# Performance work log

Hardware: AMD Instinct MI355X
Metric: run time of the kernel (lower is better)

Reference implementation:

```python
import jax, jax.numpy as jnp
import numpy as np

B, H, W, C = 8, 64, 64, 64


def setup_inputs() -> dict:
    key = jax.random.key(0)
    ks = jax.random.split(key, 9)
    s = 1.0 / np.sqrt(C)
    return {
        "x": jax.random.normal(ks[0], (B, H, W, C), dtype=jnp.float32),
        "wq": jax.random.uniform(ks[1], (C, C), jnp.float32, -s, s),
        "bq": jax.random.uniform(ks[2], (C,), jnp.float32, -s, s),
        "wk": jax.random.uniform(ks[3], (C, C), jnp.float32, -s, s),
        "bk": jax.random.uniform(ks[4], (C,), jnp.float32, -s, s),
        "wv": jax.random.uniform(ks[5], (C, C), jnp.float32, -s, s),
        "bv": jax.random.uniform(ks[6], (C,), jnp.float32, -s, s),
        "wp": jax.random.uniform(ks[7], (C, C), jnp.float32, -s, s),
        "bp": jax.random.uniform(ks[8], (C,), jnp.float32, -s, s),
    }


def reference(x, wq, bq, wk, bk, wv, bv, wp, bp):
    b, h, w, c = x.shape
    n = h * w
    xf = x.reshape(b, n, c)
    scale = c ** (-0.5)
    q = xf @ wq.T + bq  # [B,N,C]
    k = xf @ wk.T + bk
    v = xf @ wv.T + bv
    center_idx = (h // 2) * w + (w // 2)
    central = q[:, center_idx, :][:, None, :]           # [B,1,C]
    qb = jnp.broadcast_to(central, (b, n, c))           # rank-1 broadcast query
    pos = jnp.arange(n)
    dist = jnp.sqrt(((pos // w - h // 2) ** 2 + (pos % w - w // 2) ** 2).astype(jnp.float32))
    weights = jnp.exp(1.0 - dist)                       # [N]
    qw = qb * weights[None, :, None]
    attn = jnp.einsum('bnc,bmc->bnm', qw, k) * scale    # dense [B,N,N] (memory-bound)
    attn = jax.nn.softmax(attn, axis=-1)
    out = jnp.einsum('bnm,bmc->bnc', attn, v)
    out = out @ wp.T + bp
    return out.reshape(b, h, w, c)
```

## Files before the change

kernel.cpp:

```cpp
#include <hip/hip_runtime.h>

#define BB 8
#define NN 4096
#define CC 64
#define CENTER (32*64 + 32)
#define MS 64
#define RR (NN/MS)
#define GE 32
#define XPAD 68
#define CUT 64

struct Geom {
    short gid[2049];
    short g2d2[64];
    int ng;
};

constexpr Geom makeGeom() {
    Geom t{};
    bool occ[2049] = {};
    for (int y = 0; y < 64; ++y)
        for (int x = 0; x < 64; ++x) {
            int dy = y - 32, dx = x - 32;
            occ[dy*dy + dx*dx] = true;
        }
    int g = 0;
    for (int i = 0; i < CUT; ++i) {
        if (occ[i]) { t.gid[i] = (short)g; t.g2d2[g] = (short)i; ++g; }
        else t.gid[i] = (short)-1;
    }
    t.ng = g;
    for (int i = CUT; i <= 2048; ++i) t.gid[i] = occ[i] ? (short)g : (short)-1;
    return t;
}

constexpr int NGN = makeGeom().ng;
static_assert(NGN + 1 <= GE, "group padding");
static_assert(GE == 32, "decode assumes GE=32");
static_assert(MS * RR == NN, "geometry");
__constant__ Geom GEOM = makeGeom();

constexpr int OFF_PART = 0;
constexpr int OFF_ZP   = OFF_PART + BB*MS*GE*CC;
constexpr int OFF_OG   = OFF_ZP + BB*MS*GE;

#define FMA4(A, E, V) do { (A).x += (E)*(V).x; (A).y += (E)*(V).y; \
                           (A).z += (E)*(V).z; (A).w += (E)*(V).w; } while(0)

__global__ __launch_bounds__(256) void k_main(
    const float* __restrict__ x,
    const float* __restrict__ wq, const float* __restrict__ bq,
    const float* __restrict__ wk, const float* __restrict__ bk,
    float* __restrict__ part, float* __restrict__ zpart)
{
    __shared__ __align__(16) float xs[RR*XPAD];
    __shared__ float qs[CC];
    __shared__ float us[CC];
    __shared__ __align__(16) float ss[RR];
    __shared__ float ts_s;

    const int tid = threadIdx.x;
    const int b   = blockIdx.x & 7;
    const int ms  = blockIdx.x >> 3;
    const int m0  = ms * RR;

    float4 xr[4];
    const float4* x4 = (const float4*)x + ((size_t)b*NN + m0)*16;
    #pragma unroll
    for (int k = 0; k < 4; ++k) xr[k] = x4[tid + 256*k];

    if (tid < CC) {
        const float* xc = x + ((size_t)b*NN + CENTER)*CC;
        const float* wr = wq + tid*CC;
        float a0 = bq[tid], a1 = 0.f, a2 = 0.f, a3 = 0.f;
        #pragma unroll
        for (int i = 0; i < CC; i += 4) {
            a0 += xc[i+0]*wr[i+0]; a1 += xc[i+1]*wr[i+1];
            a2 += xc[i+2]*wr[i+2]; a3 += xc[i+3]*wr[i+3];
        }
        qs[tid] = a0+a1+a2+a3;
    }
    #pragma unroll
    for (int k = 0; k < 4; ++k) {
        const int idx = tid + 256*k;
        *(float4*)&xs[(idx >> 4)*XPAD + (idx & 15)*4] = xr[k];
    }
    __syncthreads();

    if (tid < CC) {
        float a0=0.f,a1=0.f,a2=0.f,a3=0.f;
        #pragma unroll
        for (int j = 0; j < CC; j += 4) {
            a0 += qs[j+0]*wk[(j+0)*CC + tid];
            a1 += qs[j+1]*wk[(j+1)*CC + tid];
            a2 += qs[j+2]*wk[(j+2)*CC + tid];
            a3 += qs[j+3]*wk[(j+3)*CC + tid];
        }
        us[tid] = a0+a1+a2+a3;
    } else if (tid == CC) {
        float a = 0.f;
        for (int j = 0; j < CC; ++j) a += qs[j]*bk[j];
        ts_s = a;
    }
    __syncthreads();

    if (tid < 2*RR) {
        const int r = tid >> 1, h = tid & 1;
        const float* xrow = &xs[r*XPAD + h*32];
        const float* uh = &us[h*32];
        float a0=0.f,a1=0.f,a2=0.f,a3=0.f;
        #pragma unroll
        for (int i = 0; i < 32; i += 4) {
            a0 += xrow[i+0]*uh[i+0]; a1 += xrow[i+1]*uh[i+1];
            a2 += xrow[i+2]*uh[i+2]; a3 += xrow[i+3]*uh[i+3];
        }
        float p = a0+a1+a2+a3;
        p += __shfl_xor(p, 1, 64);
        if (h == 0) ss[r] = (p + ts_s) * 0.125f;
    }
    __syncthreads();

    const int g  = tid >> 3;
    const int i0 = (tid & 7) * 8;
    const float wg = (g < NGN) ? __expf(1.f - sqrtf((float)GEOM.g2d2[g])) : 0.f;
    float4 y0 = make_float4(0.f,0.f,0.f,0.f), y1 = make_float4(0.f,0.f,0.f,0.f);
    float z = 0.f;
    #pragma unroll 4
    for (int r4 = 0; r4 < RR; r4 += 4) {
        const float4 s4 = *(const float4*)&ss[r4];
        float e;
        e = __expf(wg*s4.x); z += e;
        FMA4(y0, e, *(const float4*)&xs[(r4+0)*XPAD + i0]);
        FMA4(y1, e, *(const float4*)&xs[(r4+0)*XPAD + i0 + 4]);
        e = __expf(wg*s4.y); z += e;
        FMA4(y0, e, *(const float4*)&xs[(r4+1)*XPAD + i0]);
        FMA4(y1, e, *(const float4*)&xs[(r4+1)*XPAD + i0 + 4]);
        e = __expf(wg*s4.z); z += e;
        FMA4(y0, e, *(const float4*)&xs[(r4+2)*XPAD + i0]);
        FMA4(y1, e, *(const float4*)&xs[(r4+2)*XPAD + i0 + 4]);
        e = __expf(wg*s4.w); z += e;
        FMA4(y0, e, *(const float4*)&xs[(r4+3)*XPAD + i0]);
        FMA4(y1, e, *(const float4*)&xs[(r4+3)*XPAD + i0 + 4]);
    }
    float4* p4 = (float4*)part + ((size_t)((b*MS + ms)*GE + g)*CC + i0)/4;
    p4[0] = y0; p4[1] = y1;
    if ((tid & 7) == 0) zpart[(b*MS + ms)*GE + g] = z;
}

__global__ __launch_bounds__(256) void k_final(
    const float* __restrict__ part, const float* __restrict__ zpart,
    const float* __restrict__ wv, const float* __restrict__ bv,
    const float* __restrict__ wp, const float* __restrict__ bp,
    float* __restrict__ og)
{
    __shared__ float yred[4*CC];
    __shared__ float ysh[CC];
    __shared__ float hsh[CC];
    __shared__ float zsh;

    const int tid = threadIdx.x;
    const int b = blockIdx.x >> 5, g = blockIdx.x & 31;
    const int i = tid & 63, q = tid >> 6;

    float a = 0.f;
    #pragma unroll
    for (int j = 0; j < MS/4; ++j) {
        const int ms = q*(MS/4) + j;
        a += part[((size_t)(b*MS + ms)*GE + g)*CC + i];
    }
    yred[q*CC + i] = a;

    float zv = 0.f;
    if (tid < 64) {
        zv = zpart[(b*MS + tid)*GE + g];
        zv += __shfl_xor(zv, 1, 64);
        zv += __shfl_xor(zv, 2, 64);
        zv += __shfl_xor(zv, 4, 64);
        zv += __shfl_xor(zv, 8, 64);
        zv += __shfl_xor(zv, 16, 64);
        zv += __shfl_xor(zv, 32, 64);
        if (tid == 0) zsh = zv;
    }
    __syncthreads();
    if (tid < CC)
        ysh[tid] = yred[tid] + yred[CC+tid] + yred[2*CC+tid] + yred[3*CC+tid];
    __syncthreads();
    if (tid < CC) {
        const float* wr = wv + tid*CC;
        float a0=0.f,a1=0.f,a2=0.f,a3=0.f;
        #pragma unroll
        for (int j = 0; j < CC; j += 4) {
            a0 += wr[j+0]*ysh[j+0]; a1 += wr[j+1]*ysh[j+1];
            a2 += wr[j+2]*ysh[j+2]; a3 += wr[j+3]*ysh[j+3];
        }
        hsh[tid] = (a0+a1+a2+a3)/zsh + bv[tid];
    }
    __syncthreads();
    if (tid < CC) {
        const float* wr = wp + tid*CC;
        float a0=bp[tid],a1=0.f,a2=0.f,a3=0.f;
        #pragma unroll
        for (int j = 0; j < CC; j += 4) {
            a0 += wr[j+0]*hsh[j+0]; a1 += wr[j+1]*hsh[j+1];
            a2 += wr[j+2]*hsh[j+2]; a3 += wr[j+3]*hsh[j+3];
        }
        og[((size_t)b*GE + g)*CC + tid] = a0+a1+a2+a3;
    }
}

__global__ __launch_bounds__(256) void k_out(
    const float* __restrict__ og, float* __restrict__ out)
{
    const int i4 = blockIdx.x * 256 + threadIdx.x;
    const int c4 = i4 & 15;
    const int n  = (i4 >> 4) & (NN - 1);
    const int bb = i4 >> 16;
    const int dy = (n >> 6) - 32, dx = (n & 63) - 32;
    const int g  = GEOM.gid[dy*dy + dx*dx];
    ((float4*)out)[i4] = ((const float4*)og)[(size_t)(bb*GE + g)*16 + c4];
}

extern "C" void kernel_launch(void* const* d_in, const int* in_sizes, int n_in,
                              void* d_out, int out_size, void* d_ws, size_t ws_size,
                              hipStream_t stream) {
    const float* x  = (const float*)d_in[0];
    const float* wq = (const float*)d_in[1];
    const float* bq = (const float*)d_in[2];
    const float* wk = (const float*)d_in[3];
    const float* bk = (const float*)d_in[4];
    const float* wv = (const float*)d_in[5];
    const float* bv = (const float*)d_in[6];
    const float* wp = (const float*)d_in[7];
    const float* bp = (const float*)d_in[8];
    float* ws = (float*)d_ws;

    k_main<<<MS*8, 256, 0, stream>>>(x, wq, bq, wk, bk,
                                     ws + OFF_PART, ws + OFF_ZP);
    k_final<<<BB*GE, 256, 0, stream>>>(ws + OFF_PART, ws + OFF_ZP,
                                       wv, bv, wp, bp, ws + OFF_OG);
    k_out<<<2048, 256, 0, stream>>>(ws + OFF_OG, (float*)d_out);
}
```

Baseline: 89.21 us.

## Fuse output scatter into final kernel via precomputed group position jobs

```diff
diff --git a/kernel.cpp b/kernel.cpp
--- a/kernel.cpp
+++ b/kernel.cpp
@@ -8,7 +8,9 @@
 #define RR (NN/MS)
 #define GE 32
 #define XPAD 68
+#define ESP 68
 #define CUT 64
+#define CHUNK 128
 
 struct Geom {
     short gid[2049];
@@ -40,9 +42,49 @@
 static_assert(MS * RR == NN, "geometry");
 __constant__ Geom GEOM = makeGeom();
 
+struct Jobs {
+    int nj;
+    short jg[96];
+    short jstart[96];
+    short jlen[96];
+    unsigned short pos[NN];
+};
+
+constexpr Jobs makeJobs() {
+    Jobs J{};
+    Geom gm = makeGeom();
+    int cnt[NGN + 1] = {};
+    for (int n = 0; n < NN; ++n) {
+        int dy = (n >> 6) - 32, dx = (n & 63) - 32;
+        cnt[gm.gid[dy*dy + dx*dx]]++;
+    }
+    int off[NGN + 2]; off[0] = 0;
+    for (int g = 0; g <= NGN; ++g) off[g+1] = off[g] + cnt[g];
+    int cur[NGN + 1];
+    for (int g = 0; g <= NGN; ++g) cur[g] = off[g];
+    for (int n = 0; n < NN; ++n) {
+        int dy = (n >> 6) - 32, dx = (n & 63) - 32;
+        int g = gm.gid[dy*dy + dx*dx];
+        J.pos[cur[g]++] = (unsigned short)n;
+    }
+    int j = 0;
+    for (int g = 0; g <= NGN; ++g)
+        for (int s = off[g]; s < off[g+1]; s += CHUNK) {
+            int L = off[g+1] - s;
+            J.jg[j] = (short)g; J.jstart[j] = (short)s;
+            J.jlen[j] = (short)(L < CHUNK ? L : CHUNK);
+            ++j;
+        }
+    J.nj = j;
+    return J;
+}
+
+constexpr int NJ = makeJobs().nj;
+static_assert(NJ <= 96, "job table overflow");
+__constant__ Jobs JOBS = makeJobs();
+
 constexpr int OFF_PART = 0;
 constexpr int OFF_ZP   = OFF_PART + BB*MS*GE*CC;
-constexpr int OFF_OG   = OFF_ZP + BB*MS*GE;
 
 #define FMA4(A, E, V) do { (A).x += (E)*(V).x; (A).y += (E)*(V).y; \
                            (A).z += (E)*(V).z; (A).w += (E)*(V).w; } while(0)
@@ -54,31 +96,33 @@
     float* __restrict__ part, float* __restrict__ zpart)
 {
     __shared__ __align__(16) float xs[RR*XPAD];
-    __shared__ float qs[CC];
-    __shared__ float us[CC];
+    __shared__ __align__(16) float Es[GE*ESP];
+    __shared__ __align__(16) float qp[4][CC];
+    __shared__ __align__(16) float qs[CC];
+    __shared__ __align__(16) float us[CC];
     __shared__ __align__(16) float ss[RR];
+    __shared__ float wgs[GE];
     __shared__ float ts_s;
 
     const int tid = threadIdx.x;
     const int b   = blockIdx.x & 7;
     const int ms  = blockIdx.x >> 3;
     const int m0  = ms * RR;
+    const int c   = tid & 63;
+    const int qd  = tid >> 6;
 
     float4 xr[4];
     const float4* x4 = (const float4*)x + ((size_t)b*NN + m0)*16;
     #pragma unroll
     for (int k = 0; k < 4; ++k) xr[k] = x4[tid + 256*k];
 
-    if (tid < CC) {
-        const float* xc = x + ((size_t)b*NN + CENTER)*CC;
-        const float* wr = wq + tid*CC;
-        float a0 = bq[tid], a1 = 0.f, a2 = 0.f, a3 = 0.f;
-        #pragma unroll
-        for (int i = 0; i < CC; i += 4) {
-            a0 += xc[i+0]*wr[i+0]; a1 += xc[i+1]*wr[i+1];
-            a2 += xc[i+2]*wr[i+2]; a3 += xc[i+3]*wr[i+3];
-        }
-        qs[tid] = a0+a1+a2+a3;
+    {
+        const float* xc = x + ((size_t)b*NN + CENTER)*CC + qd*16;
+        const float* wr = wq + c*CC + qd*16;
+        float a = (qd == 0) ? bq[c] : 0.f;
+        #pragma unroll
+        for (int i = 0; i < 16; ++i) a += xc[i]*wr[i];
+        qp[qd][c] = a;
     }
     #pragma unroll
     for (int k = 0; k < 4; ++k) {
@@ -87,92 +131,116 @@
     }
     __syncthreads();
 
-    if (tid < CC) {
-        float a0=0.f,a1=0.f,a2=0.f,a3=0.f;
-        #pragma unroll
-        for (int j = 0; j < CC; j += 4) {
-            a0 += qs[j+0]*wk[(j+0)*CC + tid];
-            a1 += qs[j+1]*wk[(j+1)*CC + tid];
-            a2 += qs[j+2]*wk[(j+2)*CC + tid];
-            a3 += qs[j+3]*wk[(j+3)*CC + tid];
+    if (tid < CC) qs[tid] = qp[0][tid] + qp[1][tid] + qp[2][tid] + qp[3][tid];
+    if (tid < GE) wgs[tid] = (tid < NGN) ? __expf(1.f - sqrtf((float)GEOM.g2d2[tid])) : 0.f;
+    __syncthreads();
+
+    {
+        const float* wc = wk + (qd*16)*CC + c;
+        float a = 0.f;
+        #pragma unroll
+        for (int j = 0; j < 16; ++j) a += qs[qd*16 + j] * wc[j*CC];
+        qp[qd][c] = a;
+    }
+    if (tid >= 64 && tid < 128) {
+        const int l = tid - 64;
+        float p = qs[l] * bk[l];
+        p += __shfl_xor(p, 1, 64);
+        p += __shfl_xor(p, 2, 64);
+        p += __shfl_xor(p, 4, 64);
+        p += __shfl_xor(p, 8, 64);
+        p += __shfl_xor(p, 16, 64);
+        p += __shfl_xor(p, 32, 64);
+        if (l == 0) ts_s = p;
+    }
+    __syncthreads();
+    if (tid < CC) us[tid] = qp[0][tid] + qp[1][tid] + qp[2][tid] + qp[3][tid];
+    __syncthreads();
+
+    {
+        const int r = tid >> 2, h = tid & 3;
+        const float4* xp = (const float4*)&xs[r*XPAD + h*16];
+        const float4* up = (const float4*)&us[h*16];
+        const float4 x0 = xp[0], x1 = xp[1], x2 = xp[2], x3 = xp[3];
+        const float4 u0 = up[0], u1 = up[1], u2 = up[2], u3 = up[3];
+        float p = x0.x*u0.x + x0.y*u0.y + x0.z*u0.z + x0.w*u0.w
+                + x1.x*u1.x + x1.y*u1.y + x1.z*u1.z + x1.w*u1.w
+                + x2.x*u2.x + x2.y*u2.y + x2.z*u2.z + x2.w*u2.w
+                + x3.x*u3.x + x3.y*u3.y + x3.z*u3.z + x3.w*u3.w;
+        p += __shfl_xor(p, 1, 64);
+        p += __shfl_xor(p, 2, 64);
+        if (h == 0) ss[r] = (p + ts_s) * 0.125f;
+    }
+    __syncthreads();
+
+    {
+        const int r = c;
+        const float sr = ss[r];
+        #pragma unroll
+        for (int gg = 0; gg < 8; ++gg) {
+            const int g = qd*8 + gg;
+            Es[g*ESP + r] = __expf(wgs[g] * sr);
         }
-        us[tid] = a0+a1+a2+a3;
-    } else if (tid == CC) {
-        float a = 0.f;
-        for (int j = 0; j < CC; ++j) a += qs[j]*bk[j];
-        ts_s = a;
-    }
-    __syncthreads();
-
-    if (tid < 2*RR) {
-        const int r = tid >> 1, h = tid & 1;
-        const float* xrow = &xs[r*XPAD + h*32];
-        const float* uh = &us[h*32];
-        float a0=0.f,a1=0.f,a2=0.f,a3=0.f;
-        #pragma unroll
-        for (int i = 0; i < 32; i += 4) {
-            a0 += xrow[i+0]*uh[i+0]; a1 += xrow[i+1]*uh[i+1];
-            a2 += xrow[i+2]*uh[i+2]; a3 += xrow[i+3]*uh[i+3];
-        }
-        float p = a0+a1+a2+a3;
-        p += __shfl_xor(p, 1, 64);
-        if (h == 0) ss[r] = (p + ts_s) * 0.125f;
-    }
-    __syncthreads();
-
-    const int g  = tid >> 3;
-    const int i0 = (tid & 7) * 8;
-    const float wg = (g < NGN) ? __expf(1.f - sqrtf((float)GEOM.g2d2[g])) : 0.f;
+    }
+    __syncthreads();
+
+    if (tid < 128) {
+        const int g = tid >> 2, rq = tid & 3;
+        const float4* ep = (const float4*)&Es[g*ESP + rq*16];
+        const float4 e0 = ep[0], e1 = ep[1], e2 = ep[2], e3 = ep[3];
+        float z = (e0.x+e0.y+e0.z+e0.w) + (e1.x+e1.y+e1.z+e1.w)
+                + (e2.x+e2.y+e2.z+e2.w) + (e3.x+e3.y+e3.z+e3.w);
+        z += __shfl_xor(z, 1, 64);
+        z += __shfl_xor(z, 2, 64);
+        if (rq == 0) zpart[(b*MS + ms)*GE + g] = z;
+    }
+
+    const int gp = tid >> 4;
+    const int i0 = (tid & 15) * 4;
+    const int gA = 2*gp;
     float4 y0 = make_float4(0.f,0.f,0.f,0.f), y1 = make_float4(0.f,0.f,0.f,0.f);
-    float z = 0.f;
     #pragma unroll 4
     for (int r4 = 0; r4 < RR; r4 += 4) {
-        const float4 s4 = *(const float4*)&ss[r4];
-        float e;
-        e = __expf(wg*s4.x); z += e;
-        FMA4(y0, e, *(const float4*)&xs[(r4+0)*XPAD + i0]);
-        FMA4(y1, e, *(const float4*)&xs[(r4+0)*XPAD + i0 + 4]);
-        e = __expf(wg*s4.y); z += e;
-        FMA4(y0, e, *(const float4*)&xs[(r4+1)*XPAD + i0]);
-        FMA4(y1, e, *(const float4*)&xs[(r4+1)*XPAD + i0 + 4]);
-        e = __expf(wg*s4.z); z += e;
-        FMA4(y0, e, *(const float4*)&xs[(r4+2)*XPAD + i0]);
-        FMA4(y1, e, *(const float4*)&xs[(r4+2)*XPAD + i0 + 4]);
-        e = __expf(wg*s4.w); z += e;
-        FMA4(y0, e, *(const float4*)&xs[(r4+3)*XPAD + i0]);
-        FMA4(y1, e, *(const float4*)&xs[(r4+3)*XPAD + i0 + 4]);
-    }
-    float4* p4 = (float4*)part + ((size_t)((b*MS + ms)*GE + g)*CC + i0)/4;
-    p4[0] = y0; p4[1] = y1;
-    if ((tid & 7) == 0) zpart[(b*MS + ms)*GE + g] = z;
-}
-
-__global__ __launch_bounds__(256) void k_final(
+        const float4 eA = *(const float4*)&Es[gA*ESP + r4];
+        const float4 eB = *(const float4*)&Es[(gA+1)*ESP + r4];
+        float4 xa;
+        xa = *(const float4*)&xs[(r4+0)*XPAD + i0]; FMA4(y0, eA.x, xa); FMA4(y1, eB.x, xa);
+        xa = *(const float4*)&xs[(r4+1)*XPAD + i0]; FMA4(y0, eA.y, xa); FMA4(y1, eB.y, xa);
+        xa = *(const float4*)&xs[(r4+2)*XPAD + i0]; FMA4(y0, eA.z, xa); FMA4(y1, eB.z, xa);
+        xa = *(const float4*)&xs[(r4+3)*XPAD + i0]; FMA4(y0, eA.w, xa); FMA4(y1, eB.w, xa);
+    }
+    float4* p4 = (float4*)part + ((size_t)((b*MS + ms)*GE + gA)*CC + i0)/4;
+    p4[0]    = y0;
+    p4[CC/4] = y1;
+}
+
+__global__ __launch_bounds__(256) void k_fin(
     const float* __restrict__ part, const float* __restrict__ zpart,
     const float* __restrict__ wv, const float* __restrict__ bv,
     const float* __restrict__ wp, const float* __restrict__ bp,
-    float* __restrict__ og)
+    float* __restrict__ out)
 {
     __shared__ float yred[4*CC];
     __shared__ float ysh[CC];
     __shared__ float hsh[CC];
+    __shared__ __align__(16) float og_l[CC];
     __shared__ float zsh;
 
     const int tid = threadIdx.x;
-    const int b = blockIdx.x >> 5, g = blockIdx.x & 31;
-    const int i = tid & 63, q = tid >> 6;
+    const int b   = blockIdx.x & 7;
+    const int j   = blockIdx.x >> 3;
+    const int g   = JOBS.jg[j];
+    const int c   = tid & 63;
+    const int q   = tid >> 6;
 
     float a = 0.f;
     #pragma unroll
-    for (int j = 0; j < MS/4; ++j) {
-        const int ms = q*(MS/4) + j;
-        a += part[((size_t)(b*MS + ms)*GE + g)*CC + i];
-    }
-    yred[q*CC + i] = a;
-
-    float zv = 0.f;
+    for (int m = 0; m < MS/4; ++m)
+        a += part[((size_t)((b*MS + q*(MS/4) + m)*GE + g))*CC + c];
+    yred[q*CC + c] = a;
+
     if (tid < 64) {
-        zv = zpart[(b*MS + tid)*GE + g];
+        float zv = zpart[(b*MS + tid)*GE + g];
         zv += __shfl_xor(zv, 1, 64);
         zv += __shfl_xor(zv, 2, 64);
         zv += __shfl_xor(zv, 4, 64);
@@ -182,42 +250,43 @@
         if (tid == 0) zsh = zv;
     }
     __syncthreads();
+    if (tid < CC) ysh[tid] = yred[tid] + yred[CC+tid] + yred[2*CC+tid] + yred[3*CC+tid];
+    __syncthreads();
+
+    {
+        const float* wr = wv + c*CC + q*16;
+        const float* yp = ysh + q*16;
+        float p = 0.f;
+        #pragma unroll
+        for (int i = 0; i < 16; ++i) p += wr[i]*yp[i];
+        yred[q*CC + c] = p;
+    }
+    __syncthreads();
     if (tid < CC)
-        ysh[tid] = yred[tid] + yred[CC+tid] + yred[2*CC+tid] + yred[3*CC+tid];
-    __syncthreads();
-    if (tid < CC) {
-        const float* wr = wv + tid*CC;
-        float a0=0.f,a1=0.f,a2=0.f,a3=0.f;
-        #pragma unroll
-        for (int j = 0; j < CC; j += 4) {
-            a0 += wr[j+0]*ysh[j+0]; a1 += wr[j+1]*ysh[j+1];
-            a2 += wr[j+2]*ysh[j+2]; a3 += wr[j+3]*ysh[j+3];
-        }
-        hsh[tid] = (a0+a1+a2+a3)/zsh + bv[tid];
-    }
-    __syncthreads();
-    if (tid < CC) {
-        const float* wr = wp + tid*CC;
-        float a0=bp[tid],a1=0.f,a2=0.f,a3=0.f;
-        #pragma unroll
-        for (int j = 0; j < CC; j += 4) {
-            a0 += wr[j+0]*hsh[j+0]; a1 += wr[j+1]*hsh[j+1];
-            a2 += wr[j+2]*hsh[j+2]; a3 += wr[j+3]*hsh[j+3];
-        }
-        og[((size_t)b*GE + g)*CC + tid] = a0+a1+a2+a3;
-    }
-}
-
-__global__ __launch_bounds__(256) void k_out(
-    const float* __restrict__ og, float* __restrict__ out)
-{
-    const int i4 = blockIdx.x * 256 + threadIdx.x;
-    const int c4 = i4 & 15;
-    const int n  = (i4 >> 4) & (NN - 1);
-    const int bb = i4 >> 16;
-    const int dy = (n >> 6) - 32, dx = (n & 63) - 32;
-    const int g  = GEOM.gid[dy*dy + dx*dx];
-    ((float4*)out)[i4] = ((const float4*)og)[(size_t)(bb*GE + g)*16 + c4];
+        hsh[tid] = (yred[tid] + yred[CC+tid] + yred[2*CC+tid] + yred[3*CC+tid]) / zsh + bv[tid];
+    __syncthreads();
+
+    {
+        const float* wr = wp + c*CC + q*16;
+        const float* hp = hsh + q*16;
+        float p = 0.f;
+        #pragma unroll
+        for (int i = 0; i < 16; ++i) p += wr[i]*hp[i];
+        yred[q*CC + c] = p;
+    }
+    __syncthreads();
+    if (tid < CC)
+        og_l[tid] = yred[tid] + yred[CC+tid] + yred[2*CC+tid] + yred[3*CC+tid] + bp[tid];
+    __syncthreads();
+
+    const int start = JOBS.jstart[j], len = JOBS.jlen[j];
+    const int c4 = tid & 15;
+    const float4 val = ((const float4*)og_l)[c4];
+    float4* out4 = (float4*)out + ((size_t)b << 16);
+    for (int k = tid >> 4; k < len; k += 16) {
+        const int n = JOBS.pos[start + k];
+        out4[n*16 + c4] = val;
+    }
 }
 
 extern "C" void kernel_launch(void* const* d_in, const int* in_sizes, int n_in,
@@ -236,7 +305,6 @@
 
     k_main<<<MS*8, 256, 0, stream>>>(x, wq, bq, wk, bk,
                                      ws + OFF_PART, ws + OFF_ZP);
-    k_final<<<BB*GE, 256, 0, stream>>>(ws + OFF_PART, ws + OFF_ZP,
-                                       wv, bv, wp, bp, ws + OFF_OG);
-    k_out<<<2048, 256, 0, stream>>>(ws + OFF_OG, (float*)d_out);
-}
+    k_fin<<<NJ*8, 256, 0, stream>>>(ws + OFF_PART, ws + OFF_ZP,
+                                    wv, bv, wp, bp, (float*)d_out);
+}
```

Result: no change. 89.17 us (-0.0%).
